# Kernel optimization log

Measured on AMD Instinct MI355X. Metric: run time of the kernel, lower is better.

The kernel has to match this reference:

```python
import jax, jax.numpy as jnp
import numpy as np

N = 100000
E = 1600000
IN_N, IN_E = 128, 32
OUT_N, OUT_E = 64, 16
H = 4
NUM_CLASSES = 16
SLOPE = 0.2  # LeakyReLU negative slope (GAT default)


def _p(key, shape):
    return jax.random.normal(key, shape, dtype=jnp.float32) * 0.05


def setup_inputs() -> dict:
    key = jax.random.key(0)
    ks = jax.random.split(key, 20)
    inp = {
        'nfeat': jax.random.normal(ks[0], (N, IN_N), dtype=jnp.float32),
        'efeat': jax.random.normal(ks[1], (E, IN_E), dtype=jnp.float32),
        'src': jax.random.randint(ks[2], (E,), 0, N, dtype=jnp.int32),
        'dst': jax.random.randint(ks[3], (E,), 0, N, dtype=jnp.int32),
        # ---- conv1 params (EGATConv: in 128/32 -> out 64/16, 4 heads) ----
        'W1_ni': _p(ks[4], (IN_N, H * OUT_E)),
        'W1_fij': _p(ks[5], (IN_E, H * OUT_E)),
        'W1_nj': _p(ks[6], (IN_N, H * OUT_E)),
        'b1_edge': jnp.zeros((H * OUT_E,), jnp.float32),
        'W1_node': _p(ks[7], (IN_N, H * OUT_N)),
        'b1_node': jnp.zeros((H * OUT_N,), jnp.float32),
        'attn1': _p(ks[8], (H, OUT_E)),
        # ---- conv2 params (in 64/16 -> out num_classes / 1, 4 heads) ----
        'W2_ni': _p(ks[9], (OUT_N, H * 1)),
        'W2_fij': _p(ks[10], (OUT_E, H * 1)),
        'W2_nj': _p(ks[11], (OUT_N, H * 1)),
        'b2_edge': jnp.zeros((H * 1,), jnp.float32),
        'W2_node': _p(ks[12], (OUT_N, H * NUM_CLASSES)),
        'b2_node': jnp.zeros((H * NUM_CLASSES,), jnp.float32),
        'attn2': _p(ks[13], (H, 1)),
    }
    return inp


def egat_conv(nf, ef, src, dst, W_ni, W_fij, W_nj, b_edge, W_node, b_node, attn,
              heads, out_e, out_n):
    n = nf.shape[0]
    # edge feature projection: gather node projections onto edges
    f_ni = nf @ W_ni                                  # [N, H*oe]
    f_nj = nf @ W_nj                                  # [N, H*oe]
    f = f_ni[src] + (ef @ W_fij) + f_nj[dst] + b_edge  # [E, H*oe]
    f = jnp.where(f > 0, f, SLOPE * f)                 # LeakyReLU
    f = f.reshape(-1, heads, out_e)                    # [E, H, oe]
    # attention logits per head
    e = jnp.einsum('ehd,hd->eh', f, attn)              # [E, H]
    # segment softmax over destination neighborhoods
    m = jax.ops.segment_max(e, dst, num_segments=n)    # [N, H]
    a = jnp.exp(e - m[dst])
    s = jax.ops.segment_sum(a, dst, num_segments=n)    # [N, H]
    a = a / jnp.where(s == 0, 1.0, s)[dst]             # [E, H]
    # message passing: attention-weighted source features, scatter-sum to dst
    ft = (nf @ W_node + b_node).reshape(n, heads, out_n)  # [N, H, on]
    msg = ft[src] * a[:, :, None]                         # [E, H, on]
    out = jax.ops.segment_sum(msg, dst, num_segments=n)   # [N, H, on]
    return out, f


def reference(nfeat, efeat, src, dst,
              W1_ni, W1_fij, W1_nj, b1_edge, W1_node, b1_node, attn1,
              W2_ni, W2_fij, W2_nj, b2_edge, W2_node, b2_node, attn2):
    h, fe = egat_conv(nfeat, efeat, src, dst,
                      W1_ni, W1_fij, W1_nj, b1_edge, W1_node, b1_node, attn1,
                      H, OUT_E, OUT_N)
    # ReLU between layers; average heads so dims match conv2's declared inputs
    h = jax.nn.relu(h).mean(axis=1)    # [N, OUT_N]
    fe = jax.nn.relu(fe).mean(axis=1)  # [E, OUT_E]
    out, _ = egat_conv(h, fe, src, dst,
                       W2_ni, W2_fij, W2_nj, b2_edge, W2_node, b2_node, attn2,
                       H, 1, NUM_CLASSES)
    return out  # [N, H, NUM_CLASSES]
```

## Files before the change

kernel.cpp:

```cpp
#include <hip/hip_runtime.h>

#define SLOPE 0.2f
#define NPB 16

typedef float vf4 __attribute__((ext_vector_type(4)));
typedef float vf2 __attribute__((ext_vector_type(2)));
typedef _Float16 vh2 __attribute__((ext_vector_type(2)));
typedef _Float16 vh4 __attribute__((ext_vector_type(4)));

__device__ __forceinline__ float bcast_lane(float v, int k) {
    return __uint_as_float(__builtin_amdgcn_readlane(__float_as_uint(v), k));
}
__device__ __forceinline__ float dpp_sum16(float x) {
    x += __uint_as_float(__builtin_amdgcn_update_dpp(
        0, (int)__float_as_uint(x), 0x111, 0xf, 0xf, true));
    x += __uint_as_float(__builtin_amdgcn_update_dpp(
        0, (int)__float_as_uint(x), 0x112, 0xf, 0xf, true));
    x += __uint_as_float(__builtin_amdgcn_update_dpp(
        0, (int)__float_as_uint(x), 0x114, 0xf, 0xf, true));
    x += __uint_as_float(__builtin_amdgcn_update_dpp(
        0, (int)__float_as_uint(x), 0x118, 0xf, 0xf, true));
    return x;
}


__global__ __launch_bounds__(256) void k_deg(
    const int* __restrict__ dst, int* __restrict__ deg, int E)
{
    const int e = blockIdx.x * 256 + threadIdx.x;
    if (e < E) atomicAdd(&deg[dst[e]], 1);
}

__global__ __launch_bounds__(256) void k_scan1(
    const int* __restrict__ deg, int* __restrict__ bsum, int n)
{
    const int t = threadIdx.x;
    const int i0 = blockIdx.x * 1024 + t * 4;
    int s = 0;
#pragma unroll
    for (int j = 0; j < 4; j++) if (i0 + j < n) s += deg[i0 + j];
#pragma unroll
    for (int d = 1; d < 64; d <<= 1) s += __shfl_xor(s, d, 64);
    __shared__ int ws[4];
    if ((t & 63) == 0) ws[t >> 6] = s;
    __syncthreads();
    if (t == 0) bsum[blockIdx.x] = ws[0] + ws[1] + ws[2] + ws[3];
}

__global__ __launch_bounds__(64) void k_scan2(
    int* __restrict__ bsum, int* __restrict__ offs, int nb, int n)
{
    const int lane = threadIdx.x;
    int carry = 0;
    for (int base = 0; base < nb; base += 64) {
        const int i = base + lane;
        const int v = (i < nb) ? bsum[i] : 0;
        int x = v;
#pragma unroll
        for (int d = 1; d < 64; d <<= 1) {
            const int y = __shfl_up(x, d, 64);
            if (lane >= d) x += y;
        }
        if (i < nb) bsum[i] = carry + x - v;
        carry += __shfl(x, 63, 64);
    }
    if (lane == 0) offs[n] = carry;
}

__global__ __launch_bounds__(256) void k_scan3(
    const int* __restrict__ deg, const int* __restrict__ bsum,
    int* __restrict__ offs, int* __restrict__ cursor, int n)
{
    const int t = threadIdx.x;
    const int lane = t & 63, wid = t >> 6;
    const int i0 = blockIdx.x * 1024 + t * 4;
    const int d0 = (i0     < n) ? deg[i0]     : 0;
    const int d1 = (i0 + 1 < n) ? deg[i0 + 1] : 0;
    const int d2 = (i0 + 2 < n) ? deg[i0 + 2] : 0;
    const int d3 = (i0 + 3 < n) ? deg[i0 + 3] : 0;
    const int v = d0 + d1 + d2 + d3;
    int x = v;
#pragma unroll
    for (int d = 1; d < 64; d <<= 1) {
        const int y = __shfl_up(x, d, 64);
        if (lane >= d) x += y;
    }
    __shared__ int ws[4];
    if (lane == 63) ws[wid] = x;
    __syncthreads();
    int wbase = 0;
    for (int q = 0; q < wid; q++) wbase += ws[q];
    int excl = bsum[blockIdx.x] + wbase + (x - v);
    if (i0     < n) { offs[i0]     = excl; cursor[i0]     = excl; }
    excl += d0;
    if (i0 + 1 < n) { offs[i0 + 1] = excl; cursor[i0 + 1] = excl; }
    excl += d1;
    if (i0 + 2 < n) { offs[i0 + 2] = excl; cursor[i0 + 2] = excl; }
    excl += d2;
    if (i0 + 3 < n) { offs[i0 + 3] = excl; cursor[i0 + 3] = excl; }
}

__global__ __launch_bounds__(256) void k_scatter(
    const int* __restrict__ src, const int* __restrict__ dst,
    int* __restrict__ cursor, int* __restrict__ srcs, int* __restrict__ eid,
    int E)
{
    const int e = blockIdx.x * 256 + threadIdx.x;
    if (e >= E) return;
    const int p = atomicAdd(&cursor[dst[e]], 1);
    srcs[p] = src[e];
    eid[p] = e;
}

__global__ __launch_bounds__(256) void k_nodeproj1(
    const float* __restrict__ nf, const float* __restrict__ Wni,
    const float* __restrict__ Wnj,
    _Float16* __restrict__ fni16, _Float16* __restrict__ fnj16,
    _Float16* __restrict__ nf16, int n)
{
    __shared__ float s[128][20];
    const int t = threadIdx.x;
    const int node0 = blockIdx.x * NPB;
    for (int i = 0; i < 8; i++) {
        const int idx = i * 256 + t;
        const int k = idx & 127, nl = idx >> 7;
        const int node = node0 + nl;
        const float v = (node < n) ? nf[(size_t)node * 128 + k] : 0.f;
        s[k][nl] = v;
        if (node < n) nf16[(size_t)node * 128 + k] = (_Float16)v;
    }
    __syncthreads();
    const int lane = t & 63;
    const int w4 = (t >> 6) * 4;
    float ai[4] = {0, 0, 0, 0}, aj[4] = {0, 0, 0, 0};
#pragma unroll 4
    for (int k = 0; k < 128; k++) {
        const float wi = Wni[(size_t)k * 64 + lane];
        const float wj = Wnj[(size_t)k * 64 + lane];
        const float4 sv = *(const float4*)&s[k][w4];
        const float sl[4] = {sv.x, sv.y, sv.z, sv.w};
#pragma unroll
        for (int nn = 0; nn < 4; nn++) {
            ai[nn] = fmaf(wi, sl[nn], ai[nn]);
            aj[nn] = fmaf(wj, sl[nn], aj[nn]);
        }
    }
#pragma unroll
    for (int nn = 0; nn < 4; nn++) {
        const int node = node0 + w4 + nn;
        if (node < n) {
            fni16[(size_t)node * 64 + lane] = (_Float16)ai[nn];
            fnj16[(size_t)node * 64 + lane] = (_Float16)aj[nn];
        }
    }
}

__global__ __launch_bounds__(256, 4) void k_l1(
    const int* __restrict__ offs, const int* __restrict__ srcs,
    const int* __restrict__ eid, const float* __restrict__ ef,
    const _Float16* __restrict__ nf16, const _Float16* __restrict__ fni16,
    const _Float16* __restrict__ fnj16, const float* __restrict__ Wfij,
    const float* __restrict__ bedge, const float* __restrict__ attn,
    const float* __restrict__ Wfij2,
    _Float16* __restrict__ g2s, _Float16* __restrict__ zbuf, int n)
{
    const int lane = threadIdx.x & 63;
    const int node = __builtin_amdgcn_readfirstlane(blockIdx.x * 4 + (threadIdx.x >> 6));
    if (node >= n) return;
    const int beg = offs[node], end = offs[node + 1];
    const float fjb = (float)fnj16[(size_t)node * 64 + lane] + bedge[lane];
    const float at = attn[lane];
    const float w2f = Wfij2[(lane & 15) * 4 + (lane >> 4)];
    float wf[32];
#pragma unroll
    for (int k = 0; k < 32; k++) wf[k] = Wfij[k * 64 + lane];
#pragma unroll
    for (int k = 0; k < 32; k++) asm volatile("" : "+v"(wf[k]));

    float s0 = 0.f, s1 = 0.f, s2 = 0.f, s3 = 0.f;
    vf2 z0 = {0.f, 0.f}, z1 = {0.f, 0.f}, z2 = {0.f, 0.f}, z3 = {0.f, 0.f};

    for (int base = beg; base < end; base += 64) {
        const int rem = end - base;
        const int cnt = (rem < 64) ? rem : 64;
        const int idx = base + ((lane < cnt) ? lane : (cnt - 1));
        const int spv = srcs[idx];
        const int edv = eid[idx];
#pragma unroll 2
        for (int it = 0; it < cnt; ++it) {
            const int sp = __builtin_amdgcn_readlane(spv, it);
            const int ed = __builtin_amdgcn_readlane(edv, it);
            const vf4* __restrict__ efr =
                (const vf4*)(ef + ((size_t)(unsigned)ed << 5));
            const vf4 q0 = __builtin_nontemporal_load(efr + 0);
            const vf4 q1 = __builtin_nontemporal_load(efr + 1);
            const vf4 q2 = __builtin_nontemporal_load(efr + 2);
            const vf4 q3 = __builtin_nontemporal_load(efr + 3);
            const vf4 q4 = __builtin_nontemporal_load(efr + 4);
            const vf4 q5 = __builtin_nontemporal_load(efr + 5);
            const vf4 q6 = __builtin_nontemporal_load(efr + 6);
            const vf4 q7 = __builtin_nontemporal_load(efr + 7);
            float f0 = (float)fni16[(size_t)(unsigned)sp * 64 + lane] + fjb;
            f0 = fmaf(q0.x, wf[0],  f0); f0 = fmaf(q0.y, wf[1],  f0);
            f0 = fmaf(q0.z, wf[2],  f0); f0 = fmaf(q0.w, wf[3],  f0);
            f0 = fmaf(q1.x, wf[4],  f0); f0 = fmaf(q1.y, wf[5],  f0);
            f0 = fmaf(q1.z, wf[6],  f0); f0 = fmaf(q1.w, wf[7],  f0);
            float f1 = q2.x * wf[8];
            f1 = fmaf(q2.y, wf[9],  f1); f1 = fmaf(q2.z, wf[10], f1);
            f1 = fmaf(q2.w, wf[11], f1); f1 = fmaf(q3.x, wf[12], f1);
            f1 = fmaf(q3.y, wf[13], f1); f1 = fmaf(q3.z, wf[14], f1);
            f1 = fmaf(q3.w, wf[15], f1);
            float f2 = q4.x * wf[16];
            f2 = fmaf(q4.y, wf[17], f2); f2 = fmaf(q4.z, wf[18], f2);
            f2 = fmaf(q4.w, wf[19], f2); f2 = fmaf(q5.x, wf[20], f2);
            f2 = fmaf(q5.y, wf[21], f2); f2 = fmaf(q5.z, wf[22], f2);
            f2 = fmaf(q5.w, wf[23], f2);
            float f3 = q6.x * wf[24];
            f3 = fmaf(q6.y, wf[25], f3); f3 = fmaf(q6.z, wf[26], f3);
            f3 = fmaf(q6.w, wf[27], f3); f3 = fmaf(q7.x, wf[28], f3);
            f3 = fmaf(q7.y, wf[29], f3); f3 = fmaf(q7.z, wf[30], f3);
            f3 = fmaf(q7.w, wf[31], f3);
            const float f = (f0 + f1) + (f2 + f3);
            const float fl = (f > 0.f) ? f : SLOPE * f;
            float r = fmaxf(fl, 0.f);
            r += __shfl_xor(r, 16, 64);
            r += __shfl_xor(r, 32, 64);
            float g = dpp_sum16(0.25f * r * w2f);
            if ((lane & 15) == 15)
                g2s[(size_t)(base + it) * 4 + (lane >> 4)] = (_Float16)g;
            const float t = dpp_sum16(fl * at);
            const float ce = __expf(t);
            const float c0 = bcast_lane(ce, 15);
            const float c1 = bcast_lane(ce, 31);
            const float c2 = bcast_lane(ce, 47);
            const float c3 = bcast_lane(ce, 63);
            const vh2 nvh = *(const vh2*)(nf16 + (size_t)(unsigned)sp * 128 + lane * 2);
            const float nvx = (float)nvh.x, nvy = (float)nvh.y;
            s0 += c0; s1 += c1; s2 += c2; s3 += c3;
            z0.x = fmaf(c0, nvx, z0.x); z0.y = fmaf(c0, nvy, z0.y);
            z1.x = fmaf(c1, nvx, z1.x); z1.y = fmaf(c1, nvy, z1.y);
            z2.x = fmaf(c2, nvx, z2.x); z2.y = fmaf(c2, nvy, z2.y);
            z3.x = fmaf(c3, nvx, z3.x); z3.y = fmaf(c3, nvy, z3.y);
        }
    }
    const float i0 = (s0 > 0.f) ? 1.f / s0 : 0.f;
    const float i1 = (s1 > 0.f) ? 1.f / s1 : 0.f;
    const float i2 = (s2 > 0.f) ? 1.f / s2 : 0.f;
    const float i3 = (s3 > 0.f) ? 1.f / s3 : 0.f;
    _Float16* zb = zbuf + (size_t)node * 512;
    vh2 o;
    o.x = (_Float16)(z0.x * i0); o.y = (_Float16)(z0.y * i0);
    *(vh2*)(zb + 0   + lane * 2) = o;
    o.x = (_Float16)(z1.x * i1); o.y = (_Float16)(z1.y * i1);
    *(vh2*)(zb + 128 + lane * 2) = o;
    o.x = (_Float16)(z2.x * i2); o.y = (_Float16)(z2.y * i2);
    *(vh2*)(zb + 256 + lane * 2) = o;
    o.x = (_Float16)(z3.x * i3); o.y = (_Float16)(z3.y * i3);
    *(vh2*)(zb + 384 + lane * 2) = o;
}

__global__ __launch_bounds__(256) void k_zproj(
    const _Float16* __restrict__ zbuf, const int* __restrict__ offs,
    const float* __restrict__ Wnode, const float* __restrict__ bnode,
    float* __restrict__ hbuf, int n)
{
    __shared__ float s[512][20];
    const int t = threadIdx.x;
    const int node0 = blockIdx.x * NPB;
    for (int i = 0; i < 16; i++) {
        const int idx = i * 256 + t;
        const int nl = idx >> 8, kk = (idx & 255) * 2;
        const int node = node0 + nl;
        vh2 v = {0.f, 0.f};
        if (node < n) v = *(const vh2*)(zbuf + (size_t)node * 512 + kk);
        s[kk][nl]     = (float)v.x;
        s[kk + 1][nl] = (float)v.y;
    }
    __syncthreads();
    const int lane = t & 63;
    const int w4 = (t >> 6) * 4;
    bool zf[4];
    float hb[4] = {0, 0, 0, 0};
#pragma unroll
    for (int nn = 0; nn < 4; nn++) {
        const int node = node0 + w4 + nn;
        zf[nn] = (node < n) && (offs[node] < offs[node + 1]);
    }
#pragma unroll
    for (int h = 0; h < 4; h++) {
        float acc[4];
        const float bv = bnode[h * 64 + lane];
#pragma unroll
        for (int nn = 0; nn < 4; nn++) acc[nn] = zf[nn] ? bv : 0.f;
#pragma unroll 4
        for (int k = 0; k < 128; k++) {
            const float wv = Wnode[(size_t)k * 256 + h * 64 + lane];
            const float4 sv = *(const float4*)&s[h * 128 + k][w4];
            acc[0] = fmaf(wv, sv.x, acc[0]);
            acc[1] = fmaf(wv, sv.y, acc[1]);
            acc[2] = fmaf(wv, sv.z, acc[2]);
            acc[3] = fmaf(wv, sv.w, acc[3]);
        }
#pragma unroll
        for (int nn = 0; nn < 4; nn++) hb[nn] += fmaxf(acc[nn], 0.f);
    }
#pragma unroll
    for (int nn = 0; nn < 4; nn++) {
        const int node = node0 + w4 + nn;
        if (node < n) hbuf[(size_t)node * 64 + lane] = 0.25f * hb[nn];
    }
}

__global__ __launch_bounds__(256) void k_nodeproj2(
    const float* __restrict__ hbuf, const float* __restrict__ Wni,
    const float* __restrict__ Wnj, const float* __restrict__ Wnode,
    const float* __restrict__ bnode,
    float* __restrict__ fni2, float* __restrict__ fnj2,
    _Float16* __restrict__ ft2h, int n)
{
    __shared__ float sh[4][64];
    const int lane = threadIdx.x & 63, w = threadIdx.x >> 6;
    const int node = blockIdx.x * 4 + w;
    const int nc = (node < n) ? node : (n - 1);
    const float v = hbuf[(size_t)nc * 64 + lane];
    sh[w][lane] = v;
    __syncthreads();
    float acc = bnode[lane];
#pragma unroll 4
    for (int k = 0; k < 64; k++) acc = fmaf(sh[w][k], Wnode[k * 64 + lane], acc);
    float pi[4], pj[4];
#pragma unroll
    for (int h = 0; h < 4; h++) { pi[h] = v * Wni[lane * 4 + h]; pj[h] = v * Wnj[lane * 4 + h]; }
#pragma unroll
    for (int mk = 1; mk < 64; mk <<= 1) {
#pragma unroll
        for (int h = 0; h < 4; h++) {
            pi[h] += __shfl_xor(pi[h], mk, 64);
            pj[h] += __shfl_xor(pj[h], mk, 64);
        }
    }
    if (node < n) {
        ft2h[(size_t)node * 64 + lane] = (_Float16)acc;
        if (lane == 0) {
            *(float4*)(fni2 + (size_t)node * 4) = make_float4(pi[0], pi[1], pi[2], pi[3]);
            *(float4*)(fnj2 + (size_t)node * 4) = make_float4(pj[0], pj[1], pj[2], pj[3]);
        }
    }
}

__global__ __launch_bounds__(256) void k_l2(
    const int* __restrict__ offs, const int* __restrict__ srcs,
    const _Float16* __restrict__ g2s, const float* __restrict__ fni2,
    const float* __restrict__ fnj2, const _Float16* __restrict__ ft2h,
    const float* __restrict__ bedge2, const float* __restrict__ attn2,
    float* __restrict__ out, int n)
{
    const int lane = threadIdx.x & 63;
    const int node = __builtin_amdgcn_readfirstlane(blockIdx.x * 4 + (threadIdx.x >> 6));
    if (node >= n) return;
    const int beg = offs[node], end = offs[node + 1];
    const int h = lane >> 4;
    const float base_ = fnj2[(size_t)node * 4 + h] + bedge2[h];
    const float at = attn2[h];
    float s = 0.f, acc = 0.f;
    for (int base = beg; base < end; base += 64) {
        const int rem = end - base;
        const int cnt = (rem < 64) ? rem : 64;
        const int idx = base + ((lane < cnt) ? lane : (cnt - 1));
        const int spv = srcs[idx];
#pragma unroll 2
        for (int it = 0; it < cnt; ++it) {
            const int sp = __builtin_amdgcn_readlane(spv, it);
            const int p = base + it;
            const vh4 gq = *(const vh4*)(g2s + (size_t)p * 4);
            const float4 fq = *(const float4*)(fni2 + (size_t)(unsigned)sp * 4);
            const float gh = (float)((h == 0) ? gq.x : (h == 1) ? gq.y : (h == 2) ? gq.z : gq.w);
            const float fh = (h == 0) ? fq.x : (h == 1) ? fq.y : (h == 2) ? fq.z : fq.w;
            const float f = base_ + fh + gh;
            const float fl = (f > 0.f) ? f : SLOPE * f;
            const float c = __expf(fl * at);
            s += c;
            const float ftv = (float)ft2h[(size_t)(unsigned)sp * 64 + lane];
            acc = fmaf(c, ftv, acc);
        }
    }
    out[(size_t)node * 64 + lane] = (s > 0.f) ? acc / s : 0.f;
}

extern "C" void kernel_launch(void* const* d_in, const int* in_sizes, int n_in,
                              void* d_out, int out_size, void* d_ws, size_t ws_size,
                              hipStream_t stream)
{
    const float* nfeat  = (const float*)d_in[0];
    const float* efeat  = (const float*)d_in[1];
    const int*   src    = (const int*)d_in[2];
    const int*   dst    = (const int*)d_in[3];
    const float* W1ni   = (const float*)d_in[4];
    const float* W1fij  = (const float*)d_in[5];
    const float* W1nj   = (const float*)d_in[6];
    const float* b1e    = (const float*)d_in[7];
    const float* W1node = (const float*)d_in[8];
    const float* b1n    = (const float*)d_in[9];
    const float* attn1  = (const float*)d_in[10];
    const float* W2ni   = (const float*)d_in[11];
    const float* W2fij  = (const float*)d_in[12];
    const float* W2nj   = (const float*)d_in[13];
    const float* b2e    = (const float*)d_in[14];
    const float* W2node = (const float*)d_in[15];
    const float* b2n    = (const float*)d_in[16];
    const float* attn2  = (const float*)d_in[17];
    const int n = in_sizes[0] / 128;
    const int E = in_sizes[2];
    float* out = (float*)d_out;

    char* w = (char*)d_ws;
    auto alloc = [&](size_t bytes) {
        char* p = w; w += (bytes + 255) & ~(size_t)255; return p;
    };
    _Float16* zbuf  = (_Float16*)alloc((size_t)n * 512 * 2);
    _Float16* g2s   = (_Float16*)alloc((size_t)E * 4 * 2);
    _Float16* fni16 = (_Float16*)alloc((size_t)n * 64 * 2);
    _Float16* fnj16 = (_Float16*)alloc((size_t)n * 64 * 2);
    _Float16* nf16  = (_Float16*)alloc((size_t)n * 128 * 2);
    _Float16* ft2h  = (_Float16*)alloc((size_t)n * 64 * 2);
    float*    hbuf  = (float*)alloc((size_t)n * 64 * 4);
    int*      deg   = (int*)alloc((size_t)n * 4);
    int*      offs  = (int*)alloc((size_t)(n + 1) * 4);
    int*      curs  = (int*)alloc((size_t)n * 4);
    int*      srcs  = (int*)alloc((size_t)E * 4);
    int*      eid   = (int*)alloc((size_t)E * 4);
    float*    fni2  = (float*)alloc((size_t)n * 4 * 4);
    float*    fnj2  = (float*)alloc((size_t)n * 4 * 4);
    const int nb = (n + 1023) / 1024;
    int*      bsum  = (int*)alloc((size_t)nb * 4);

    hipMemsetAsync(deg, 0, (size_t)n * 4, stream);
    k_deg<<<(E + 255) / 256, 256, 0, stream>>>(dst, deg, E);
    k_scan1<<<nb, 256, 0, stream>>>(deg, bsum, n);
    k_scan2<<<1, 64, 0, stream>>>(bsum, offs, nb, n);
    k_scan3<<<nb, 256, 0, stream>>>(deg, bsum, offs, curs, n);
    k_scatter<<<(E + 255) / 256, 256, 0, stream>>>(src, dst, curs, srcs, eid, E);

    k_nodeproj1<<<(n + NPB - 1) / NPB, 256, 0, stream>>>(
        nfeat, W1ni, W1nj, fni16, fnj16, nf16, n);
    k_l1<<<(n + 3) / 4, 256, 0, stream>>>(offs, srcs, eid, efeat, nf16,
                                          fni16, fnj16, W1fij, b1e, attn1,
                                          W2fij, g2s, zbuf, n);
    k_zproj<<<(n + NPB - 1) / NPB, 256, 0, stream>>>(zbuf, offs, W1node, b1n,
                                                     hbuf, n);
    k_nodeproj2<<<(n + 3) / 4, 256, 0, stream>>>(hbuf, W2ni, W2nj, W2node, b2n,
                                                 fni2, fnj2, ft2h, n);
    k_l2<<<(n + 3) / 4, 256, 0, stream>>>(offs, srcs, g2s, fni2, fnj2, ft2h,
                                          b2e, attn2, out, n);
}
```

Before: 1.074 ms.

## Convert edge features to fp16 up front, use fdot2, pack src/eid arrays

The degree-count kernel now also converts the 1.6M x 32 edge-feature matrix to fp16. k_l1 then gathers half-size edge rows and computes the edge projection with packed fp16 dot2 instructions and fp16 weights. The srcs and eid arrays are interleaved into one int2 array so each edge needs a single load, hbuf is stored as fp16, and the unroll in k_l2 is raised. The extra conversion pass reads the fp32 edge features once and writes fp16, so total traffic may not drop much, and precision in the edge projection is reduced.

New measurement: 1.053 ms. No clear change (-1.9%).

```diff
diff --git a/kernel.cpp b/kernel.cpp
--- a/kernel.cpp
+++ b/kernel.cpp
@@ -7,6 +7,7 @@
 typedef float vf2 __attribute__((ext_vector_type(2)));
 typedef _Float16 vh2 __attribute__((ext_vector_type(2)));
 typedef _Float16 vh4 __attribute__((ext_vector_type(4)));
+typedef _Float16 vh8 __attribute__((ext_vector_type(8)));
 
 __device__ __forceinline__ float bcast_lane(float v, int k) {
     return __uint_as_float(__builtin_amdgcn_readlane(__float_as_uint(v), k));
@@ -24,11 +25,23 @@
 }
 
 
-__global__ __launch_bounds__(256) void k_deg(
-    const int* __restrict__ dst, int* __restrict__ deg, int E)
-{
-    const int e = blockIdx.x * 256 + threadIdx.x;
-    if (e < E) atomicAdd(&deg[dst[e]], 1);
+__global__ __launch_bounds__(256) void k_deg_cvt(
+    const int* __restrict__ dst, int* __restrict__ deg,
+    const float* __restrict__ ef, _Float16* __restrict__ ef16, int E)
+{
+    const size_t i = (size_t)blockIdx.x * 256 + threadIdx.x;
+    if (i < (size_t)E) atomicAdd(&deg[dst[i]], 1);
+    const size_t b = i * 8;
+    if (b < (size_t)E * 32) {
+        const vf4 a0 = __builtin_nontemporal_load((const vf4*)(ef + b));
+        const vf4 a1 = __builtin_nontemporal_load((const vf4*)(ef + b + 4));
+        vh8 o;
+        o[0] = (_Float16)a0.x; o[1] = (_Float16)a0.y;
+        o[2] = (_Float16)a0.z; o[3] = (_Float16)a0.w;
+        o[4] = (_Float16)a1.x; o[5] = (_Float16)a1.y;
+        o[6] = (_Float16)a1.z; o[7] = (_Float16)a1.w;
+        __builtin_nontemporal_store(o, (vh8*)(ef16 + b));
+    }
 }
 
 __global__ __launch_bounds__(256) void k_scan1(
@@ -102,14 +115,12 @@
 
 __global__ __launch_bounds__(256) void k_scatter(
     const int* __restrict__ src, const int* __restrict__ dst,
-    int* __restrict__ cursor, int* __restrict__ srcs, int* __restrict__ eid,
-    int E)
+    int* __restrict__ cursor, int2* __restrict__ se, int E)
 {
     const int e = blockIdx.x * 256 + threadIdx.x;
     if (e >= E) return;
     const int p = atomicAdd(&cursor[dst[e]], 1);
-    srcs[p] = src[e];
-    eid[p] = e;
+    se[p] = make_int2(src[e], e);
 }
 
 __global__ __launch_bounds__(256) void k_nodeproj1(
@@ -156,8 +167,8 @@
 }
 
 __global__ __launch_bounds__(256, 4) void k_l1(
-    const int* __restrict__ offs, const int* __restrict__ srcs,
-    const int* __restrict__ eid, const float* __restrict__ ef,
+    const int* __restrict__ offs, const int2* __restrict__ se,
+    const _Float16* __restrict__ ef16,
     const _Float16* __restrict__ nf16, const _Float16* __restrict__ fni16,
     const _Float16* __restrict__ fnj16, const float* __restrict__ Wfij,
     const float* __restrict__ bedge, const float* __restrict__ attn,
@@ -171,55 +182,53 @@
     const float fjb = (float)fnj16[(size_t)node * 64 + lane] + bedge[lane];
     const float at = attn[lane];
     const float w2f = Wfij2[(lane & 15) * 4 + (lane >> 4)];
-    float wf[32];
-#pragma unroll
-    for (int k = 0; k < 32; k++) wf[k] = Wfij[k * 64 + lane];
-#pragma unroll
-    for (int k = 0; k < 32; k++) asm volatile("" : "+v"(wf[k]));
+    vh2 wf[16];
+#pragma unroll
+    for (int j = 0; j < 16; j++) {
+        vh2 p;
+        p.x = (_Float16)Wfij[(2 * j) * 64 + lane];
+        p.y = (_Float16)Wfij[(2 * j + 1) * 64 + lane];
+        wf[j] = p;
+    }
+#pragma unroll
+    for (int j = 0; j < 16; j++) asm volatile("" : "+v"(wf[j]));
 
     float s0 = 0.f, s1 = 0.f, s2 = 0.f, s3 = 0.f;
     vf2 z0 = {0.f, 0.f}, z1 = {0.f, 0.f}, z2 = {0.f, 0.f}, z3 = {0.f, 0.f};
 
+#define PAIR(u, j) (vh2){(u)[2 * (j)], (u)[2 * (j) + 1]}
     for (int base = beg; base < end; base += 64) {
         const int rem = end - base;
         const int cnt = (rem < 64) ? rem : 64;
         const int idx = base + ((lane < cnt) ? lane : (cnt - 1));
-        const int spv = srcs[idx];
-        const int edv = eid[idx];
+        const int2 sev = se[idx];
+        const int spv = sev.x, edv = sev.y;
 #pragma unroll 2
         for (int it = 0; it < cnt; ++it) {
             const int sp = __builtin_amdgcn_readlane(spv, it);
             const int ed = __builtin_amdgcn_readlane(edv, it);
-            const vf4* __restrict__ efr =
-                (const vf4*)(ef + ((size_t)(unsigned)ed << 5));
-            const vf4 q0 = __builtin_nontemporal_load(efr + 0);
-            const vf4 q1 = __builtin_nontemporal_load(efr + 1);
-            const vf4 q2 = __builtin_nontemporal_load(efr + 2);
-            const vf4 q3 = __builtin_nontemporal_load(efr + 3);
-            const vf4 q4 = __builtin_nontemporal_load(efr + 4);
-            const vf4 q5 = __builtin_nontemporal_load(efr + 5);
-            const vf4 q6 = __builtin_nontemporal_load(efr + 6);
-            const vf4 q7 = __builtin_nontemporal_load(efr + 7);
+            const vh8* __restrict__ er = (const vh8*)(ef16 + ((size_t)(unsigned)ed << 5));
+            const vh8 u0 = __builtin_nontemporal_load(er + 0);
+            const vh8 u1 = __builtin_nontemporal_load(er + 1);
+            const vh8 u2 = __builtin_nontemporal_load(er + 2);
+            const vh8 u3 = __builtin_nontemporal_load(er + 3);
             float f0 = (float)fni16[(size_t)(unsigned)sp * 64 + lane] + fjb;
-            f0 = fmaf(q0.x, wf[0],  f0); f0 = fmaf(q0.y, wf[1],  f0);
-            f0 = fmaf(q0.z, wf[2],  f0); f0 = fmaf(q0.w, wf[3],  f0);
-            f0 = fmaf(q1.x, wf[4],  f0); f0 = fmaf(q1.y, wf[5],  f0);
-            f0 = fmaf(q1.z, wf[6],  f0); f0 = fmaf(q1.w, wf[7],  f0);
-            float f1 = q2.x * wf[8];
-            f1 = fmaf(q2.y, wf[9],  f1); f1 = fmaf(q2.z, wf[10], f1);
-            f1 = fmaf(q2.w, wf[11], f1); f1 = fmaf(q3.x, wf[12], f1);
-            f1 = fmaf(q3.y, wf[13], f1); f1 = fmaf(q3.z, wf[14], f1);
-            f1 = fmaf(q3.w, wf[15], f1);
-            float f2 = q4.x * wf[16];
-            f2 = fmaf(q4.y, wf[17], f2); f2 = fmaf(q4.z, wf[18], f2);
-            f2 = fmaf(q4.w, wf[19], f2); f2 = fmaf(q5.x, wf[20], f2);
-            f2 = fmaf(q5.y, wf[21], f2); f2 = fmaf(q5.z, wf[22], f2);
-            f2 = fmaf(q5.w, wf[23], f2);
-            float f3 = q6.x * wf[24];
-            f3 = fmaf(q6.y, wf[25], f3); f3 = fmaf(q6.z, wf[26], f3);
-            f3 = fmaf(q6.w, wf[27], f3); f3 = fmaf(q7.x, wf[28], f3);
-            f3 = fmaf(q7.y, wf[29], f3); f3 = fmaf(q7.z, wf[30], f3);
-            f3 = fmaf(q7.w, wf[31], f3);
+            f0 = __builtin_amdgcn_fdot2(PAIR(u0, 0), wf[0],  f0, false);
+            f0 = __builtin_amdgcn_fdot2(PAIR(u0, 1), wf[1],  f0, false);
+            f0 = __builtin_amdgcn_fdot2(PAIR(u0, 2), wf[2],  f0, false);
+            f0 = __builtin_amdgcn_fdot2(PAIR(u0, 3), wf[3],  f0, false);
+            float f1 = __builtin_amdgcn_fdot2(PAIR(u1, 0), wf[4], 0.f, false);
+            f1 = __builtin_amdgcn_fdot2(PAIR(u1, 1), wf[5],  f1, false);
+            f1 = __builtin_amdgcn_fdot2(PAIR(u1, 2), wf[6],  f1, false);
+            f1 = __builtin_amdgcn_fdot2(PAIR(u1, 3), wf[7],  f1, false);
+            float f2 = __builtin_amdgcn_fdot2(PAIR(u2, 0), wf[8], 0.f, false);
+            f2 = __builtin_amdgcn_fdot2(PAIR(u2, 1), wf[9],  f2, false);
+            f2 = __builtin_amdgcn_fdot2(PAIR(u2, 2), wf[10], f2, false);
+            f2 = __builtin_amdgcn_fdot2(PAIR(u2, 3), wf[11], f2, false);
+            float f3 = __builtin_amdgcn_fdot2(PAIR(u3, 0), wf[12], 0.f, false);
+            f3 = __builtin_amdgcn_fdot2(PAIR(u3, 1), wf[13], f3, false);
+            f3 = __builtin_amdgcn_fdot2(PAIR(u3, 2), wf[14], f3, false);
+            f3 = __builtin_amdgcn_fdot2(PAIR(u3, 3), wf[15], f3, false);
             const float f = (f0 + f1) + (f2 + f3);
             const float fl = (f > 0.f) ? f : SLOPE * f;
             float r = fmaxf(fl, 0.f);
@@ -243,6 +252,7 @@
             z3.x = fmaf(c3, nvx, z3.x); z3.y = fmaf(c3, nvy, z3.y);
         }
     }
+#undef PAIR
     const float i0 = (s0 > 0.f) ? 1.f / s0 : 0.f;
     const float i1 = (s1 > 0.f) ? 1.f / s1 : 0.f;
     const float i2 = (s2 > 0.f) ? 1.f / s2 : 0.f;
@@ -262,7 +272,7 @@
 __global__ __launch_bounds__(256) void k_zproj(
     const _Float16* __restrict__ zbuf, const int* __restrict__ offs,
     const float* __restrict__ Wnode, const float* __restrict__ bnode,
-    float* __restrict__ hbuf, int n)
+    _Float16* __restrict__ hbuf16, int n)
 {
     __shared__ float s[512][20];
     const int t = threadIdx.x;
@@ -307,12 +317,12 @@
 #pragma unroll
     for (int nn = 0; nn < 4; nn++) {
         const int node = node0 + w4 + nn;
-        if (node < n) hbuf[(size_t)node * 64 + lane] = 0.25f * hb[nn];
+        if (node < n) hbuf16[(size_t)node * 64 + lane] = (_Float16)(0.25f * hb[nn]);
     }
 }
 
 __global__ __launch_bounds__(256) void k_nodeproj2(
-    const float* __restrict__ hbuf, const float* __restrict__ Wni,
+    const _Float16* __restrict__ hbuf16, const float* __restrict__ Wni,
     const float* __restrict__ Wnj, const float* __restrict__ Wnode,
     const float* __restrict__ bnode,
     float* __restrict__ fni2, float* __restrict__ fnj2,
@@ -322,7 +332,7 @@
     const int lane = threadIdx.x & 63, w = threadIdx.x >> 6;
     const int node = blockIdx.x * 4 + w;
     const int nc = (node < n) ? node : (n - 1);
-    const float v = hbuf[(size_t)nc * 64 + lane];
+    const float v = (float)hbuf16[(size_t)nc * 64 + lane];
     sh[w][lane] = v;
     __syncthreads();
     float acc = bnode[lane];
@@ -349,7 +359,7 @@
 }
 
 __global__ __launch_bounds__(256) void k_l2(
-    const int* __restrict__ offs, const int* __restrict__ srcs,
+    const int* __restrict__ offs, const int2* __restrict__ se,
     const _Float16* __restrict__ g2s, const float* __restrict__ fni2,
     const float* __restrict__ fnj2, const _Float16* __restrict__ ft2h,
     const float* __restrict__ bedge2, const float* __restrict__ attn2,
@@ -367,8 +377,8 @@
         const int rem = end - base;
         const int cnt = (rem < 64) ? rem : 64;
         const int idx = base + ((lane < cnt) ? lane : (cnt - 1));
-        const int spv = srcs[idx];
-#pragma unroll 2
+        const int spv = se[idx].x;
+#pragma unroll 4
         for (int it = 0; it < cnt; ++it) {
             const int sp = __builtin_amdgcn_readlane(spv, it);
             const int p = base + it;
@@ -417,39 +427,40 @@
     auto alloc = [&](size_t bytes) {
         char* p = w; w += (bytes + 255) & ~(size_t)255; return p;
     };
+    _Float16* ef16  = (_Float16*)alloc((size_t)E * 32 * 2);
     _Float16* zbuf  = (_Float16*)alloc((size_t)n * 512 * 2);
     _Float16* g2s   = (_Float16*)alloc((size_t)E * 4 * 2);
     _Float16* fni16 = (_Float16*)alloc((size_t)n * 64 * 2);
     _Float16* fnj16 = (_Float16*)alloc((size_t)n * 64 * 2);
     _Float16* nf16  = (_Float16*)alloc((size_t)n * 128 * 2);
     _Float16* ft2h  = (_Float16*)alloc((size_t)n * 64 * 2);
-    float*    hbuf  = (float*)alloc((size_t)n * 64 * 4);
+    _Float16* hbuf16= (_Float16*)alloc((size_t)n * 64 * 2);
     int*      deg   = (int*)alloc((size_t)n * 4);
     int*      offs  = (int*)alloc((size_t)(n + 1) * 4);
     int*      curs  = (int*)alloc((size_t)n * 4);
-    int*      srcs  = (int*)alloc((size_t)E * 4);
-    int*      eid   = (int*)alloc((size_t)E * 4);
+    int2*     se    = (int2*)alloc((size_t)E * 8);
     float*    fni2  = (float*)alloc((size_t)n * 4 * 4);
     float*    fnj2  = (float*)alloc((size_t)n * 4 * 4);
     const int nb = (n + 1023) / 1024;
     int*      bsum  = (int*)alloc((size_t)nb * 4);
 
     hipMemsetAsync(deg, 0, (size_t)n * 4, stream);
-    k_deg<<<(E + 255) / 256, 256, 0, stream>>>(dst, deg, E);
+    const int cvtBlocks = (int)(((size_t)E * 4 + 255) / 256);
+    k_deg_cvt<<<cvtBlocks, 256, 0, stream>>>(dst, deg, efeat, ef16, E);
     k_scan1<<<nb, 256, 0, stream>>>(deg, bsum, n);
     k_scan2<<<1, 64, 0, stream>>>(bsum, offs, nb, n);
     k_scan3<<<nb, 256, 0, stream>>>(deg, bsum, offs, curs, n);
-    k_scatter<<<(E + 255) / 256, 256, 0, stream>>>(src, dst, curs, srcs, eid, E);
+    k_scatter<<<(E + 255) / 256, 256, 0, stream>>>(src, dst, curs, se, E);
 
     k_nodeproj1<<<(n + NPB - 1) / NPB, 256, 0, stream>>>(
         nfeat, W1ni, W1nj, fni16, fnj16, nf16, n);
-    k_l1<<<(n + 3) / 4, 256, 0, stream>>>(offs, srcs, eid, efeat, nf16,
+    k_l1<<<(n + 3) / 4, 256, 0, stream>>>(offs, se, ef16, nf16,
                                           fni16, fnj16, W1fij, b1e, attn1,
                                           W2fij, g2s, zbuf, n);
     k_zproj<<<(n + NPB - 1) / NPB, 256, 0, stream>>>(zbuf, offs, W1node, b1n,
-                                                     hbuf, n);
-    k_nodeproj2<<<(n + 3) / 4, 256, 0, stream>>>(hbuf, W2ni, W2nj, W2node, b2n,
+                                                     hbuf16, n);
+    k_nodeproj2<<<(n + 3) / 4, 256, 0, stream>>>(hbuf16, W2ni, W2nj, W2node, b2n,
                                                  fni2, fnj2, ft2h, n);
-    k_l2<<<(n + 3) / 4, 256, 0, stream>>>(offs, srcs, g2s, fni2, fnj2, ft2h,
+    k_l2<<<(n + 3) / 4, 256, 0, stream>>>(offs, se, g2s, fni2, fnj2, ft2h,
                                           b2e, attn2, out, n);
 }
```
